# Optimization experiments

Hardware: AMD Instinct MI355X
Metric: run time of the kernel (lower is better)

The kernel has to match this reference:

```python
import jax, jax.numpy as jnp
import numpy as np

M = 16          # num_particles
EPS = 0.006


def setup_inputs() -> dict:
    key = jax.random.key(0)
    k1, k2, k3, k4 = jax.random.split(key, 4)
    B, P, O = 131072, 16, 4  # batch, pred_horizon, obs_horizon
    return {
        "ys_t": jax.random.normal(k1, (B, P, O), dtype=jnp.float32),
        "ys_r_stop": jax.random.normal(k2, (B, P, O), dtype=jnp.float32),
        "w_scale": jax.random.uniform(k3, (B,), dtype=jnp.float32),
        "time_weights": jax.random.uniform(k4, (B,), dtype=jnp.float32),
    }


def _laplace(a, b, ws, D):
    # a,b: [G, M, D]; ws: [G, M] (scale indexed by j, the first particle index)
    d = jnp.linalg.norm(a[:, :, None, :] - b[:, None, :, :], axis=-1)  # [G, M, M]
    d = jnp.maximum(d, EPS)
    return jnp.exp(-ws[:, :, None] * d / D)


def reference(ys_t, ys_r_stop, w_scale, time_weights):
    B = ys_t.shape[0]
    G = B // M
    x = ys_t.reshape(G, M, -1)        # [G, M, D]
    y = ys_r_stop.reshape(G, M, -1)   # [G, M, D]
    D = x.shape[-1]                   # pred_horizon * obs_horizon (dim_normalize)
    ws = w_scale.reshape(G, M)
    tw = time_weights.reshape(G, M)[:, 0]  # [G]
    terms = _laplace(x, x, ws, D) + _laplace(y, y, ws, D) - 2.0 * _laplace(x, y, ws, D)
    group_loss = terms.sum(axis=(1, 2)) * tw / (M * M)  # [G]
    return group_loss.sum() / G
```

## Files before the change

### kernel.cpp

```cpp
#include <hip/hip_runtime.h>


#define EPS_D 0.006f
#define DIMS 64

#define ROT(v, O) __int_as_float(__builtin_amdgcn_update_dpp(              \
        0, __float_as_int(v), 0x120 + (O), 0xF, 0xF, false))

__global__ __launch_bounds__(256, 2)
void imm_loss_kernel(const float* __restrict__ ys_t,
                     const float* __restrict__ ys_r,
                     const float* __restrict__ w_scale,
                     const float* __restrict__ time_w,
                     float* __restrict__ partials)
{
    const int tid  = threadIdx.x;
    const int lane = tid & 63;
    const int wave = tid >> 6;
    const int b    = (blockIdx.x * 4 + wave) * 64 + lane;

    float x[DIMS], y[DIMS];
    const float4* xp = reinterpret_cast<const float4*>(ys_t + (size_t)b * DIMS);
    const float4* yp = reinterpret_cast<const float4*>(ys_r + (size_t)b * DIMS);
    #pragma unroll
    for (int c = 0; c < DIMS / 4; ++c) {
        float4 v = xp[c];
        x[4*c+0] = v.x; x[4*c+1] = v.y; x[4*c+2] = v.z; x[4*c+3] = v.w;
    }
    #pragma unroll
    for (int c = 0; c < DIMS / 4; ++c) {
        float4 v = yp[c];
        y[4*c+0] = v.x; y[4*c+1] = v.y; y[4*c+2] = v.z; y[4*c+3] = v.w;
    }

    const float s_j = w_scale[b] * (1.0f / (float)DIMS);
    const float tw  = time_w[b & ~15];

    float acc = 2.0f * __expf(-s_j * EPS_D);

    {
        float d2 = 0.f;
        #pragma unroll
        for (int d = 0; d < DIMS; ++d) {
            float t = x[d] - y[d];
            d2 = fmaf(t, t, d2);
        }
        float dd = fmaxf(sqrtf(d2), EPS_D);
        acc -= 2.0f * __expf(-s_j * dd);
    }

#define FULL_O(O, W) {                                                     \
        const float s_k = ROT(s_j, O);                                     \
        float dxx = 0.f, dyy = 0.f, dxy = 0.f;                             \
        _Pragma("unroll")                                                  \
        for (int d = 0; d < DIMS; ++d) {                                   \
            float xr = ROT(x[d], O);                                       \
            float yr = ROT(y[d], O);                                       \
            float tx = xr - x[d];  dxx = fmaf(tx, tx, dxx);                \
            float ty = yr - y[d];  dyy = fmaf(ty, ty, dyy);                \
            float tz = yr - x[d];  dxy = fmaf(tz, tz, dxy);                \
        }                                                                  \
        const float ddx = fmaxf(sqrtf(dxx), EPS_D);                        \
        const float ddy = fmaxf(sqrtf(dyy), EPS_D);                        \
        const float ddz = fmaxf(sqrtf(dxy), EPS_D);                        \
        acc += (W) * (__expf(-s_j * ddx) + __expf(-s_k * ddx));            \
        acc += (W) * (__expf(-s_j * ddy) + __expf(-s_k * ddy));            \
        acc -= 2.0f * __expf(-s_j * ddz);                                  \
    }

#define XY_O(O) {                                                          \
        float dxy = 0.f;                                                   \
        _Pragma("unroll")                                                  \
        for (int d = 0; d < DIMS; ++d) {                                   \
            float tz = ROT(y[d], O) - x[d];                                \
            dxy = fmaf(tz, tz, dxy);                                       \
        }                                                                  \
        const float ddz = fmaxf(sqrtf(dxy), EPS_D);                        \
        acc -= 2.0f * __expf(-s_j * ddz);                                  \
    }

    FULL_O(1, 1.0f)
    FULL_O(2, 1.0f)
    FULL_O(3, 1.0f)
    FULL_O(4, 1.0f)
    FULL_O(5, 1.0f)
    FULL_O(6, 1.0f)
    FULL_O(7, 1.0f)
    FULL_O(8, 0.5f)
    XY_O(9)
    XY_O(10)
    XY_O(11)
    XY_O(12)
    XY_O(13)
    XY_O(14)
    XY_O(15)

    float val = acc * tw;
    #pragma unroll
    for (int off = 32; off; off >>= 1)
        val += __shfl_xor(val, off, 64);

    __shared__ float smem[4];
    if (lane == 0) smem[wave] = val;
    __syncthreads();
    if (tid == 0)
        partials[blockIdx.x] = smem[0] + smem[1] + smem[2] + smem[3];
}

__global__ void imm_reduce_kernel(const float* __restrict__ part, int n,
                                  float inv_scale, float* __restrict__ out)
{
    const int tid = threadIdx.x;
    float v = 0.f;
    for (int i = tid; i < n; i += 256) v += part[i];
    #pragma unroll
    for (int off = 32; off; off >>= 1) v += __shfl_xor(v, off, 64);
    __shared__ float s[4];
    if ((tid & 63) == 0) s[tid >> 6] = v;
    __syncthreads();
    if (tid == 0) out[0] = (s[0] + s[1] + s[2] + s[3]) * inv_scale;
}

extern "C" void kernel_launch(void* const* d_in, const int* in_sizes, int n_in,
                              void* d_out, int out_size, void* d_ws, size_t ws_size,
                              hipStream_t stream)
{
    const float* ys_t = (const float*)d_in[0];
    const float* ys_r = (const float*)d_in[1];
    const float* wsc  = (const float*)d_in[2];
    const float* twp  = (const float*)d_in[3];
    float* out      = (float*)d_out;
    float* partials = (float*)d_ws;

    const int B = in_sizes[2];
    const int G = B / 16;
    const int blocks = G / 16;

    imm_loss_kernel<<<blocks, 256, 0, stream>>>(ys_t, ys_r, wsc, twp, partials);

    const float inv_scale = 1.0f / (256.0f * (float)G);
    imm_reduce_kernel<<<1, 256, 0, stream>>>(partials, blocks, inv_scale, out);
}
```

Before: 118.3 us.

## Split each particle's 64 dims across 4 lanes with cross-lane partial reduction

Each wave now handles one group instead of four. Each particle's 64-dim vector is split across 4 lane quarters, and the partial squared distances are combined with xor-shuffles. This cuts per-thread registers from 128 to about 48, allowing launch bounds of 4 blocks per CU and more waves in flight. It also computes the y-y distance from the x-y difference plus a precomputed x-y delta, saving one subtraction per dimension. The costs are redundant sqrt/exp work in all 4 quarter-lanes, 4x more blocks and partials for the reduction kernel, and a scale factor adjusted to count each term four times.

```diff
diff --git a/kernel.cpp b/kernel.cpp
--- a/kernel.cpp
+++ b/kernel.cpp
@@ -2,12 +2,47 @@
 
 
 #define EPS_D 0.006f
-#define DIMS 64
 
 #define ROT(v, O) __int_as_float(__builtin_amdgcn_update_dpp(              \
         0, __float_as_int(v), 0x120 + (O), 0xF, 0xF, false))
 
-__global__ __launch_bounds__(256, 2)
+__device__ __forceinline__ float red4(float p) {
+    p += __shfl_xor(p, 16, 64);
+    p += __shfl_xor(p, 32, 64);
+    return p;
+}
+
+#define FULL_O(O, W) {                                                     \
+    float pxx = 0.f, pyy = 0.f, pxy = 0.f;                                 \
+    _Pragma("unroll")                                                      \
+    for (int d = 0; d < 16; ++d) {                                         \
+        float tx = ROT(xd[d], O) - xd[d];         \
+        float tz = ROT(yd[d], O) - xd[d];         \
+        float ty = tz + dl[d];                                 \
+        pxx = fmaf(tx, tx, pxx);                                           \
+        pyy = fmaf(ty, ty, pyy);                                           \
+        pxy = fmaf(tz, tz, pxy);                                           \
+    }                                                                      \
+    pxx = red4(pxx);  pyy = red4(pyy);  pxy = red4(pxy);                   \
+    const float s_k = ROT(s_j, O);                                         \
+    const float ddx = fmaxf(sqrtf(pxx), EPS_D);                            \
+    const float ddy = fmaxf(sqrtf(pyy), EPS_D);                            \
+    const float ddz = fmaxf(sqrtf(pxy), EPS_D);                            \
+    acc += (W) * (__expf(-s_j * ddx) + __expf(-s_k * ddx));                \
+    acc += (W) * (__expf(-s_j * ddy) + __expf(-s_k * ddy));                \
+    acc -= 2.0f * __expf(-s_j * ddz); }
+
+#define XY_O(O) {                                                          \
+    float pxy = 0.f;                                                       \
+    _Pragma("unroll")                                                      \
+    for (int d = 0; d < 16; ++d) {                                         \
+        float tz = ROT(yd[d], O) - xd[d];                                  \
+        pxy = fmaf(tz, tz, pxy);                                           \
+    }                                                                      \
+    pxy = red4(pxy);                                                       \
+    acc -= 2.0f * __expf(-s_j * fmaxf(sqrtf(pxy), EPS_D)); }
+
+__global__ __launch_bounds__(256, 4)
 void imm_loss_kernel(const float* __restrict__ ys_t,
                      const float* __restrict__ ys_r,
                      const float* __restrict__ w_scale,
@@ -17,66 +52,39 @@
     const int tid  = threadIdx.x;
     const int lane = tid & 63;
     const int wave = tid >> 6;
-    const int b    = (blockIdx.x * 4 + wave) * 64 + lane;
+    const int q    = lane >> 4;
+    const int j    = lane & 15;
+    const int g    = blockIdx.x * 4 + wave;
 
-    float x[DIMS], y[DIMS];
-    const float4* xp = reinterpret_cast<const float4*>(ys_t + (size_t)b * DIMS);
-    const float4* yp = reinterpret_cast<const float4*>(ys_r + (size_t)b * DIMS);
+    const size_t base = (size_t)g * 1024 + j * 64 + q * 16;
+    const float4* xp = reinterpret_cast<const float4*>(ys_t + base);
+    const float4* yp = reinterpret_cast<const float4*>(ys_r + base);
+
+    float xd[16], yd[16], dl[16];
     #pragma unroll
-    for (int c = 0; c < DIMS / 4; ++c) {
-        float4 v = xp[c];
-        x[4*c+0] = v.x; x[4*c+1] = v.y; x[4*c+2] = v.z; x[4*c+3] = v.w;
+    for (int t = 0; t < 4; ++t) {
+        float4 v = xp[t];
+        xd[4*t+0] = v.x; xd[4*t+1] = v.y; xd[4*t+2] = v.z; xd[4*t+3] = v.w;
     }
     #pragma unroll
-    for (int c = 0; c < DIMS / 4; ++c) {
-        float4 v = yp[c];
-        y[4*c+0] = v.x; y[4*c+1] = v.y; y[4*c+2] = v.z; y[4*c+3] = v.w;
+    for (int t = 0; t < 4; ++t) {
+        float4 v = yp[t];
+        yd[4*t+0] = v.x; yd[4*t+1] = v.y; yd[4*t+2] = v.z; yd[4*t+3] = v.w;
     }
+    #pragma unroll
+    for (int d = 0; d < 16; ++d) dl[d] = xd[d] - yd[d];
 
-    const float s_j = w_scale[b] * (1.0f / (float)DIMS);
-    const float tw  = time_w[b & ~15];
+    const float s_j = w_scale[g * 16 + j] * (1.0f / 64.0f);
+    const float tw  = time_w[g * 16];
 
     float acc = 2.0f * __expf(-s_j * EPS_D);
 
     {
-        float d2 = 0.f;
+        float p0 = 0.f;
         #pragma unroll
-        for (int d = 0; d < DIMS; ++d) {
-            float t = x[d] - y[d];
-            d2 = fmaf(t, t, d2);
-        }
-        float dd = fmaxf(sqrtf(d2), EPS_D);
-        acc -= 2.0f * __expf(-s_j * dd);
-    }
-
-#define FULL_O(O, W) {                                                     \
-        const float s_k = ROT(s_j, O);                                     \
-        float dxx = 0.f, dyy = 0.f, dxy = 0.f;                             \
-        _Pragma("unroll")                                                  \
-        for (int d = 0; d < DIMS; ++d) {                                   \
-            float xr = ROT(x[d], O);                                       \
-            float yr = ROT(y[d], O);                                       \
-            float tx = xr - x[d];  dxx = fmaf(tx, tx, dxx);                \
-            float ty = yr - y[d];  dyy = fmaf(ty, ty, dyy);                \
-            float tz = yr - x[d];  dxy = fmaf(tz, tz, dxy);                \
-        }                                                                  \
-        const float ddx = fmaxf(sqrtf(dxx), EPS_D);                        \
-        const float ddy = fmaxf(sqrtf(dyy), EPS_D);                        \
-        const float ddz = fmaxf(sqrtf(dxy), EPS_D);                        \
-        acc += (W) * (__expf(-s_j * ddx) + __expf(-s_k * ddx));            \
-        acc += (W) * (__expf(-s_j * ddy) + __expf(-s_k * ddy));            \
-        acc -= 2.0f * __expf(-s_j * ddz);                                  \
-    }
-
-#define XY_O(O) {                                                          \
-        float dxy = 0.f;                                                   \
-        _Pragma("unroll")                                                  \
-        for (int d = 0; d < DIMS; ++d) {                                   \
-            float tz = ROT(y[d], O) - x[d];                                \
-            dxy = fmaf(tz, tz, dxy);                                       \
-        }                                                                  \
-        const float ddz = fmaxf(sqrtf(dxy), EPS_D);                        \
-        acc -= 2.0f * __expf(-s_j * ddz);                                  \
+        for (int d = 0; d < 16; ++d) p0 = fmaf(dl[d], dl[d], p0);
+        p0 = red4(p0);
+        acc -= 2.0f * __expf(-s_j * fmaxf(sqrtf(p0), EPS_D));
     }
 
     FULL_O(1, 1.0f)
@@ -134,10 +142,10 @@
 
     const int B = in_sizes[2];
     const int G = B / 16;
-    const int blocks = G / 16;
+    const int blocks = G / 4;
 
     imm_loss_kernel<<<blocks, 256, 0, stream>>>(ys_t, ys_r, wsc, twp, partials);
 
-    const float inv_scale = 1.0f / (256.0f * (float)G);
+    const float inv_scale = 1.0f / (4.0f * 256.0f * (float)G);
     imm_reduce_kernel<<<1, 256, 0, stream>>>(partials, blocks, inv_scale, out);
 }
```

Result: no change. 118.5 us (+0.1%).
